# Kernel tuning notes

Hardware: AMD Instinct MI355X
Metric: run time of the kernel (lower is better)

The kernel has to match this reference:

```python
import jax, jax.numpy as jnp
import numpy as np

# ---- module constants (from init_kwargs) ----
VOXEL_SIZE = np.array([0.1, 0.1, 0.2], np.float32)
PC_RANGE = np.array([0.0, -40.0, -3.0, 70.4, 40.0, 1.0], np.float32)
MAX_PTS = 10            # max_points_in_voxel
MAX_VOX = 40000         # max_voxel_num (hard voxelization cap per sample)
GRID = np.round((PC_RANGE[3:] - PC_RANGE[:3]) / VOXEL_SIZE).astype(np.int32)  # [704,800,20] (x,y,z)
BIG = int(GRID[0]) * int(GRID[1]) * int(GRID[2])

PC_MIN = jnp.asarray(PC_RANGE[:3])
VSIZE = jnp.asarray(VOXEL_SIZE)
GRID_J = jnp.asarray(GRID)

B = 8
N_PER_B = 120000


def setup_inputs() -> dict:
    key = jax.random.key(0)
    k1, = jax.random.split(key, 1)
    u = jax.random.uniform(k1, (B * N_PER_B, 4), dtype=jnp.float32)
    # place points inside (and slightly around) pc_range
    x = u[:, 0] * 72.0 - 0.5
    y = u[:, 1] * 82.0 - 41.0
    z = u[:, 2] * 4.4 - 3.2
    inten = u[:, 3]
    bs_idx = jnp.repeat(jnp.arange(B, dtype=jnp.float32), N_PER_B)
    points = jnp.stack([bs_idx, x, y, z, inten], axis=1)  # [960000, 5]
    return {"points": points, "batch_size": B}


def _voxelize_one(pts):
    """Hard voxelization of one point cloud pts [N,4] -> fixed-size buffers.
    Faithful to first-come voxel ordering and per-voxel point caps."""
    N = pts.shape[0]
    idxs = jnp.arange(N, dtype=jnp.int32)
    xyz = pts[:, :3]
    c = jnp.floor((xyz - PC_MIN) / VSIZE).astype(jnp.int32)  # [N,3] (x,y,z)
    valid = jnp.all((c >= 0) & (c < GRID_J), axis=1)
    lid = (c[:, 2] * GRID[1] + c[:, 1]) * GRID[0] + c[:, 0]  # z-major linear id
    lid = jnp.where(valid, lid, BIG)

    order = jnp.argsort(lid)            # stable: within a voxel, original order kept
    lid_s = lid[order]
    is_new = jnp.concatenate([jnp.ones((1,), bool), lid_s[1:] != lid_s[:-1]])
    gid = jnp.cumsum(is_new.astype(jnp.int32)) - 1           # group id per sorted point
    starts = jax.lax.cummax(jnp.where(is_new, idxs, 0))      # group start position
    pos = idxs - starts                                      # rank inside its voxel

    g_lid = jax.ops.segment_min(lid_s, gid, num_segments=N)
    g_valid = g_lid < BIG
    first_orig = jax.ops.segment_min(order.astype(jnp.int32), gid, num_segments=N)
    # voxel slot = first-appearance rank (invalid/empty groups pushed to the end)
    first_key = jnp.where(g_valid, first_orig, N + idxs)
    perm = jnp.argsort(first_key)
    slot = jnp.zeros(N, jnp.int32).at[perm].set(idxs)

    pslot = slot[gid]
    keep = g_valid[gid] & (pslot < MAX_VOX) & (pos < MAX_PTS)
    sslot = jnp.where(keep, pslot, MAX_VOX)   # overflow bucket, sliced off
    spos = jnp.where(keep, pos, 0)
    voxels = jnp.zeros((MAX_VOX + 1, MAX_PTS, pts.shape[1]), pts.dtype)
    voxels = voxels.at[sslot, spos].set(pts[order])[:MAX_VOX]

    gcount = jax.ops.segment_sum(keep.astype(jnp.int32), gid, num_segments=N)
    gslot = jnp.where(g_valid & (slot < MAX_VOX), slot, MAX_VOX)
    num_points = jnp.zeros(MAX_VOX + 1, jnp.int32).at[gslot].set(gcount)[:MAX_VOX]

    cs = c[order]
    gz = jax.ops.segment_min(cs[:, 2], gid, num_segments=N)
    gy = jax.ops.segment_min(cs[:, 1], gid, num_segments=N)
    gx = jax.ops.segment_min(cs[:, 0], gid, num_segments=N)
    coors = jnp.full((MAX_VOX + 1, 3), -1, jnp.int32)
    coors = coors.at[gslot].set(jnp.stack([gz, gy, gx], axis=1))[:MAX_VOX]  # (z,y,x)
    return voxels, num_points, coors


def reference(points, batch_size):
    feats = points[:, 1:]
    n_per_b = feats.shape[0] // batch_size  # points constructed contiguously per sample
    pts = feats.reshape(batch_size, n_per_b, feats.shape[1])
    voxels_b, num_b, coors_b = jax.vmap(_voxelize_one)(pts)
    voxels = voxels_b.reshape(batch_size * MAX_VOX, MAX_PTS, feats.shape[1])
    num_points = num_b.reshape(-1)
    batch_col = jnp.repeat(jnp.arange(batch_size, dtype=jnp.int32), MAX_VOX)[:, None]
    coors_batch = jnp.concatenate([batch_col, coors_b.reshape(-1, 3)], axis=1)  # [b,z,y,x]
    grid_size = jnp.asarray(GRID)
    return voxels, num_points, coors_batch, grid_size
```

## Files before the change

### kernel.cpp

```cpp
#include <hip/hip_runtime.h>

#define NB        8
#define NPB       120000
#define NPTS      (NB * NPB)
#define MAX_PTS   10
#define MAX_VOX   40000
#define GX        704
#define GY        800
#define GZ        20

#define T0        (1 << 18)
#define T0MASK    (T0 - 1)
#define T1        (1 << 16)
#define T1MASK    (T1 - 1)

#define HC2       (1 << 15)
#define HMASK2    (HC2 - 1)
#define NSLOT2    (NB * HC2)

#define TILES     469
#define TILES_PAD 512
#define MBCAP     8192
#define MTILE     2048

#define EMPTY64   0xFFFFFFFFFFFFFFFFull

#define OUT_VOX   0LL
#define OUT_NUM   12800000LL
#define OUT_COOR  13120000LL
#define OUT_GRID  14400000LL

__device__ __forceinline__ bool point_cell(const float* __restrict__ p,
                                           int& cx, int& cy, int& cz) {
    cx = (int)floorf((p[1] - 0.0f)   / 0.1f);
    cy = (int)floorf((p[2] - (-40.0f)) / 0.1f);
    cz = (int)floorf((p[3] - (-3.0f))  / 0.2f);
    return (cx >= 0) & (cx < GX) & (cy >= 0) & (cy < GY) & (cz >= 0) & (cz < GZ);
}

__device__ __forceinline__ unsigned hash0(int lid) {
    return (((unsigned)lid * 2654435761u) >> 14) & T0MASK;
}
__device__ __forceinline__ unsigned hash1(int lid) {
    return (((unsigned)lid * 0x9E3779B1u) >> 16) & T1MASK;
}
__device__ __forceinline__ unsigned slab_hash(int lid) {
    return (((unsigned)lid * 2654435761u) >> 17) & HMASK2;
}

__device__ __forceinline__ void slab_insert(unsigned long long* __restrict__ base,
                                            int lid, int idx) {
    unsigned long long key = ((unsigned long long)(unsigned)lid << 32)
                           | (unsigned long long)(unsigned)idx;
    unsigned h = slab_hash(lid);
    while (true) {
        unsigned long long oo = atomicMin(base + h, key);
        if (oo == EMPTY64) break;
        if ((oo >> 32) == (key >> 32)) break;
        if (oo > key) key = oo;
        h = (h + 1) & HMASK2;
    }
}

__device__ __forceinline__ unsigned slab_find(const unsigned long long* __restrict__ base,
                                              int lid) {
    unsigned h = slab_hash(lid);
    while (true) {
        unsigned long long cur = base[h];
        if ((unsigned)(cur >> 32) == (unsigned)lid) return (unsigned)cur;
        h = (h + 1) & HMASK2;
    }
}

__device__ __forceinline__ unsigned claimer_of(const unsigned* __restrict__ tbl0,
                                               const unsigned* __restrict__ tbl1,
                                               const int* __restrict__ lid32,
                                               int b, int lid) {
    unsigned w = tbl0[b * T0 + hash0(lid)];
    if (lid32[b * NPB + (int)w] == lid) return w;
    w = tbl1[b * T1 + hash1(lid)];
    if (lid32[b * NPB + (int)w] == lid) return w;
    return 0xFFFFFFFFu;
}

__global__ void k_init(const float* __restrict__ pts, float* __restrict__ out,
                       ulonglong2* __restrict__ slab2, unsigned* __restrict__ tbl0,
                       int* __restrict__ lid32, unsigned* __restrict__ mcount) {
    int b = blockIdx.x & 7;
    int idx = (blockIdx.x >> 3) * 256 + threadIdx.x;
    if (idx < NPB) {
        int g = b * NPB + idx;
        const float* p = pts + (long long)g * 5;
        int cx, cy, cz;
        if (point_cell(p, cx, cy, cz)) {
            int lid = (cz * GY + cy) * GX + cx;
            lid32[g] = lid;
            tbl0[b * T0 + hash0(lid)] = (unsigned)idx;
        } else {
            lid32[g] = -1;
        }
    }
    int t = blockIdx.x * 256 + threadIdx.x;
    if (t < NSLOT2 / 2) {
        ulonglong2 e2; e2.x = EMPTY64; e2.y = EMPTY64;
        slab2[t] = e2;
    }
    if (t < NB) mcount[t * 16] = 0u;
    if (t == 0) {
        out[OUT_GRID + 0] = 704.f;
        out[OUT_GRID + 1] = 800.f;
        out[OUT_GRID + 2] = 20.f;
    }
}

__global__ void k_l0(const int* __restrict__ lid32, const unsigned* __restrict__ tbl0,
                     unsigned* __restrict__ tbl1, unsigned char* __restrict__ flag,
                     unsigned long long* __restrict__ slabB) {
    int b = blockIdx.x & 7;
    int idx = (blockIdx.x >> 3) * 256 + threadIdx.x;
    if (idx >= NPB) return;
    int g = b * NPB + idx;
    int lid = lid32[g];
    if (lid < 0) { flag[g] = 0; return; }
    unsigned w = tbl0[b * T0 + hash0(lid)];
    if (lid32[b * NPB + (int)w] == lid) {
        if (w == (unsigned)idx) { flag[g] = 1; return; }
        flag[g] = 0;
        slab_insert(slabB + (size_t)b * HC2, lid, idx);
        return;
    }
    tbl1[b * T1 + hash1(lid)] = (unsigned)idx;
    flag[g] = 2;
}

__global__ void k_l1(const int* __restrict__ lid32, const unsigned* __restrict__ tbl1,
                     unsigned char* __restrict__ flag,
                     unsigned long long* __restrict__ slabB) {
    int b = blockIdx.x & 7;
    int idx = (blockIdx.x >> 3) * 256 + threadIdx.x;
    if (idx >= NPB) return;
    int g = b * NPB + idx;
    if (flag[g] != 2) return;
    int lid = lid32[g];
    unsigned w = tbl1[b * T1 + hash1(lid)];
    if (lid32[b * NPB + (int)w] == lid) {
        if (w == (unsigned)idx) { flag[g] = 1; return; }
        flag[g] = 0;
        slab_insert(slabB + (size_t)b * HC2, lid, idx);
        return;
    }
    flag[g] = 0;
    slab_insert(slabB + (size_t)b * HC2, lid, idx);
}

__global__ void k_sweep(const unsigned long long* __restrict__ slabB,
                        const unsigned* __restrict__ tbl0, const unsigned* __restrict__ tbl1,
                        const int* __restrict__ lid32, unsigned char* __restrict__ flag) {
    int s = blockIdx.x * 256 + threadIdx.x;
    unsigned long long v = slabB[s];
    if (v == EMPTY64) return;
    int b = s >> 15;
    int lid = (int)(unsigned)(v >> 32);
    unsigned smin = (unsigned)v;
    unsigned cl = claimer_of(tbl0, tbl1, lid32, b, lid);
    if (cl == 0xFFFFFFFFu) {
        flag[b * NPB + (int)smin] = 1;
    } else if (smin < cl) {
        flag[b * NPB + (int)cl] = 0;
        flag[b * NPB + (int)smin] = 1;
    }
}

__global__ void k_count(const unsigned* __restrict__ flag32, const int* __restrict__ lid32,
                        const unsigned long long* __restrict__ slabB,
                        const unsigned* __restrict__ tbl0, const unsigned* __restrict__ tbl1,
                        int* __restrict__ tileSum, int2* __restrict__ mlist,
                        unsigned* __restrict__ mcount) {
    int w = blockIdx.x * 4 + ((int)threadIdx.x >> 6);
    int lane = threadIdx.x & 63;
    int b = w & 7;
    int tile = w >> 3;
    int i = tile * 64 + lane;
    unsigned x = 0u;
    if (i < NPB / 4) {
        x = flag32[b * (NPB / 4) + i];
        int4 l4 = ((const int4*)lid32)[b * (NPB / 4) + i];
        #pragma unroll
        for (int k = 0; k < 4; k++) {
            int lk = (k == 0) ? l4.x : (k == 1) ? l4.y : (k == 2) ? l4.z : l4.w;
            if (((x >> (8 * k)) & 255u) == 0u && lk >= 0) {
                unsigned smin = slab_find(slabB + (size_t)b * HC2, lk);
                unsigned cl = claimer_of(tbl0, tbl1, lid32, b, lk);
                unsigned leader = (smin < cl) ? smin : cl;
                int idx = i * 4 + k;
                unsigned m = atomicAdd(&mcount[b * 16], 1u);
                if (m < MBCAP)
                    mlist[(size_t)b * MBCAP + m] = make_int2((int)leader, idx);
            }
        }
    }
    int s = (int)((x * 0x01010101u) >> 24);
    #pragma unroll
    for (int off = 32; off; off >>= 1) s += __shfl_down(s, off);
    if (lane == 0) tileSum[b * TILES_PAD + tile] = s;
}

__global__ void k_finish(const float* __restrict__ pts, const int* __restrict__ lid32,
                         const unsigned char* __restrict__ flag,
                         const int* __restrict__ tileSum,
                         float* __restrict__ out, unsigned short* __restrict__ slotOf) {
    int b = blockIdx.x & 7;
    int tile = blockIdx.x >> 3;
    int t = threadIdx.x;

    __shared__ int sc[256];
    __shared__ int soff[TILES_PAD];
    int v0 = (2 * t     < TILES) ? tileSum[b * TILES_PAD + 2 * t]     : 0;
    int v1 = (2 * t + 1 < TILES) ? tileSum[b * TILES_PAD + 2 * t + 1] : 0;
    int w = v0 + v1;
    sc[t] = w;
    __syncthreads();
    for (int off = 1; off < 256; off <<= 1) {
        int x = sc[t];
        if (t >= off) x += sc[t - off];
        __syncthreads();
        sc[t] = x;
        __syncthreads();
    }
    int e = sc[t] - w;
    soff[2 * t] = e;
    soff[2 * t + 1] = e + v0;
    __syncthreads();

    int idx = tile * 256 + t;
    int g = b * NPB + idx;
    int f = (idx < NPB) ? (int)flag[g] : 0;
    sc[t] = f;
    __syncthreads();
    for (int off = 1; off < 256; off <<= 1) {
        int x = sc[t];
        if (t >= off) x += sc[t - off];
        __syncthreads();
        sc[t] = x;
        __syncthreads();
    }
    int rank = sc[t] - f;

    if (idx >= NPB || !f) return;

    int slot = soff[tile] + rank;
    slotOf[g] = (unsigned short)(slot < 65535 ? slot : 65535);
    if (slot >= MAX_VOX) return;
    int lid = lid32[g];
    unsigned ul = (unsigned)lid;
    unsigned cx = ul % (unsigned)GX;
    unsigned tt = ul / (unsigned)GX;
    unsigned cy = tt % (unsigned)GY;
    unsigned cz = tt / (unsigned)GY;
    long long r = (long long)b * MAX_VOX + slot;
    ((float4*)(out + OUT_COOR))[r] = make_float4((float)b, (float)cz, (float)cy, (float)cx);
    out[OUT_NUM + r] = 1.f;
    const float* p = pts + (long long)g * 5;
    float4* row = (float4*)(out + OUT_VOX) + (size_t)r * MAX_PTS;
    row[0] = make_float4(p[1], p[2], p[3], p[4]);
    float4 zf = make_float4(0.f, 0.f, 0.f, 0.f);
    #pragma unroll
    for (int i = 1; i < MAX_PTS; i++) row[i] = zf;
}

__global__ void k_multi(const float* __restrict__ pts,
                        const int2* __restrict__ mlist, const unsigned* __restrict__ mcount,
                        const unsigned short* __restrict__ slotOf,
                        float* __restrict__ out) {
    int b = blockIdx.y;
    unsigned n = mcount[b * 16];
    if (n > MBCAP) n = MBCAP;
    unsigned t = blockIdx.x * blockDim.x + threadIdx.x;
    const int2* lst = mlist + (size_t)b * MBCAP;
    bool active = (t < n);
    int2 e = active ? lst[t] : make_int2(-1, -1);
    int pos = 1;
    int same = 0;
    __shared__ int2 sm[MTILE];
    for (unsigned chunk = 0; chunk < n; chunk += MTILE) {
        unsigned m = n - chunk;
        if (m > MTILE) m = MTILE;
        for (unsigned i = threadIdx.x; i < m; i += 256)
            sm[i] = lst[chunk + i];
        __syncthreads();
        if (active) {
            #pragma unroll 4
            for (unsigned j = 0; j < m; j++) {
                int2 o = sm[j];
                if (o.x == e.x) { same++; if (o.y < e.y) pos++; }
            }
        }
        __syncthreads();
    }
    if (!active) return;
    int slot = (int)slotOf[(size_t)b * NPB + e.x];
    if (slot >= MAX_VOX) return;
    if (pos == 1) {
        int cnt = same + 1;
        out[OUT_NUM + (long long)b * MAX_VOX + slot] =
            (float)(cnt < MAX_PTS ? cnt : MAX_PTS);
    }
    if (pos >= MAX_PTS) return;
    const float* p = pts + ((long long)b * NPB + e.y) * 5;
    ((float4*)(out + OUT_VOX))[(long long)(b * MAX_VOX + slot) * MAX_PTS + pos] =
        make_float4(p[1], p[2], p[3], p[4]);
}

extern "C" void kernel_launch(void* const* d_in, const int* in_sizes, int n_in,
                              void* d_out, int out_size, void* d_ws, size_t ws_size,
                              hipStream_t stream) {
    const float* pts = (const float*)d_in[0];
    float* out = (float*)d_out;

    char* w = (char*)d_ws;
    unsigned* tbl0 = (unsigned*)w;            w += (size_t)NB * T0 * 4;
    unsigned* tbl1 = (unsigned*)w;            w += (size_t)NB * T1 * 4;
    unsigned long long* slabB = (unsigned long long*)w;
    w += (size_t)NSLOT2 * 8;
    int2* mlist = (int2*)w;  w += (size_t)NB * MBCAP * 8;
    int* lid32 = (int*)w;    w += (size_t)NPTS * 4;
    int* tileSum = (int*)w;  w += (size_t)NB * TILES_PAD * 4;
    unsigned* mcount = (unsigned*)w; w += (size_t)NB * 16 * 4;
    unsigned short* slotOf = (unsigned short*)w; w += (size_t)NPTS * 2;
    unsigned char* flag = (unsigned char*)w;  w += (size_t)NPTS;

    const int PB = TILES * NB;
    k_init<<<dim3(PB), dim3(256), 0, stream>>>(pts, out, (ulonglong2*)slabB,
                                               tbl0, lid32, mcount);
    k_l0<<<dim3(PB), dim3(256), 0, stream>>>(lid32, tbl0, tbl1, flag, slabB);
    k_l1<<<dim3(PB), dim3(256), 0, stream>>>(lid32, tbl1, flag, slabB);
    k_sweep<<<dim3(NSLOT2 / 256), dim3(256), 0, stream>>>(slabB, tbl0, tbl1, lid32, flag);
    k_count<<<dim3(TILES * NB / 4), dim3(256), 0, stream>>>((const unsigned*)flag, lid32,
                                                            slabB, tbl0, tbl1,
                                                            tileSum, mlist, mcount);
    k_finish<<<dim3(PB), dim3(256), 0, stream>>>(pts, lid32, flag, tileSum, out, slotOf);
    k_multi<<<dim3(MBCAP / 256, NB), dim3(256), 0, stream>>>(pts, mlist, mcount, slotOf, out);
}
```

Measured before the change: 156.5 us.

## Drop second-level claim table and use wavefront shuffle scans in finish

The two-level claimer hash tables are replaced by one table twice as large, which removes the k_l1 kernel launch and the second lookup in claimer_of. Points that lose in the single table now fall back to the slab hash, so that table holds more entries and its probe chains get longer. Separately, k_finish's shared-memory Hillis-Steele scans, which synchronise the block at every step, are replaced with wavefront shuffle scans plus a small per-wave sum array. The bigger table also costs more workspace memory and more random-write footprint in k_init.

```diff
diff --git a/kernel.cpp b/kernel.cpp
--- a/kernel.cpp
+++ b/kernel.cpp
@@ -9,10 +9,8 @@
 #define GY        800
 #define GZ        20
 
-#define T0        (1 << 18)
+#define T0        (1 << 19)
 #define T0MASK    (T0 - 1)
-#define T1        (1 << 16)
-#define T1MASK    (T1 - 1)
 
 #define HC2       (1 << 15)
 #define HMASK2    (HC2 - 1)
@@ -39,10 +37,7 @@
 }
 
 __device__ __forceinline__ unsigned hash0(int lid) {
-    return (((unsigned)lid * 2654435761u) >> 14) & T0MASK;
-}
-__device__ __forceinline__ unsigned hash1(int lid) {
-    return (((unsigned)lid * 0x9E3779B1u) >> 16) & T1MASK;
+    return (((unsigned)lid * 2654435761u) >> 13) & T0MASK;
 }
 __device__ __forceinline__ unsigned slab_hash(int lid) {
     return (((unsigned)lid * 2654435761u) >> 17) & HMASK2;
@@ -73,14 +68,27 @@
 }
 
 __device__ __forceinline__ unsigned claimer_of(const unsigned* __restrict__ tbl0,
-                                               const unsigned* __restrict__ tbl1,
                                                const int* __restrict__ lid32,
                                                int b, int lid) {
-    unsigned w = tbl0[b * T0 + hash0(lid)];
-    if (lid32[b * NPB + (int)w] == lid) return w;
-    w = tbl1[b * T1 + hash1(lid)];
+    unsigned w = tbl0[(size_t)b * T0 + hash0(lid)];
     if (lid32[b * NPB + (int)w] == lid) return w;
     return 0xFFFFFFFFu;
+}
+
+__device__ __forceinline__ int block_scan_excl(int v, int t, int* wsum) {
+    int lane = t & 63, wv = t >> 6;
+    int x = v;
+    #pragma unroll
+    for (int d = 1; d < 64; d <<= 1) {
+        int y = __shfl_up(x, d);
+        if (lane >= d) x += y;
+    }
+    if (lane == 63) wsum[wv] = x;
+    __syncthreads();
+    int base = 0;
+    #pragma unroll
+    for (int wj = 0; wj < 3; wj++) if (wj < wv) base += wsum[wj];
+    return base + x - v;
 }
 
 __global__ void k_init(const float* __restrict__ pts, float* __restrict__ out,
@@ -95,7 +103,7 @@
         if (point_cell(p, cx, cy, cz)) {
             int lid = (cz * GY + cy) * GX + cx;
             lid32[g] = lid;
-            tbl0[b * T0 + hash0(lid)] = (unsigned)idx;
+            tbl0[(size_t)b * T0 + hash0(lid)] = (unsigned)idx;
         } else {
             lid32[g] = -1;
         }
@@ -114,7 +122,7 @@
 }
 
 __global__ void k_l0(const int* __restrict__ lid32, const unsigned* __restrict__ tbl0,
-                     unsigned* __restrict__ tbl1, unsigned char* __restrict__ flag,
+                     unsigned char* __restrict__ flag,
                      unsigned long long* __restrict__ slabB) {
     int b = blockIdx.x & 7;
     int idx = (blockIdx.x >> 3) * 256 + threadIdx.x;
@@ -122,39 +130,19 @@
     int g = b * NPB + idx;
     int lid = lid32[g];
     if (lid < 0) { flag[g] = 0; return; }
-    unsigned w = tbl0[b * T0 + hash0(lid)];
+    unsigned w = tbl0[(size_t)b * T0 + hash0(lid)];
     if (lid32[b * NPB + (int)w] == lid) {
         if (w == (unsigned)idx) { flag[g] = 1; return; }
         flag[g] = 0;
         slab_insert(slabB + (size_t)b * HC2, lid, idx);
         return;
     }
-    tbl1[b * T1 + hash1(lid)] = (unsigned)idx;
-    flag[g] = 2;
-}
-
-__global__ void k_l1(const int* __restrict__ lid32, const unsigned* __restrict__ tbl1,
-                     unsigned char* __restrict__ flag,
-                     unsigned long long* __restrict__ slabB) {
-    int b = blockIdx.x & 7;
-    int idx = (blockIdx.x >> 3) * 256 + threadIdx.x;
-    if (idx >= NPB) return;
-    int g = b * NPB + idx;
-    if (flag[g] != 2) return;
-    int lid = lid32[g];
-    unsigned w = tbl1[b * T1 + hash1(lid)];
-    if (lid32[b * NPB + (int)w] == lid) {
-        if (w == (unsigned)idx) { flag[g] = 1; return; }
-        flag[g] = 0;
-        slab_insert(slabB + (size_t)b * HC2, lid, idx);
-        return;
-    }
     flag[g] = 0;
     slab_insert(slabB + (size_t)b * HC2, lid, idx);
 }
 
 __global__ void k_sweep(const unsigned long long* __restrict__ slabB,
-                        const unsigned* __restrict__ tbl0, const unsigned* __restrict__ tbl1,
+                        const unsigned* __restrict__ tbl0,
                         const int* __restrict__ lid32, unsigned char* __restrict__ flag) {
     int s = blockIdx.x * 256 + threadIdx.x;
     unsigned long long v = slabB[s];
@@ -162,7 +150,7 @@
     int b = s >> 15;
     int lid = (int)(unsigned)(v >> 32);
     unsigned smin = (unsigned)v;
-    unsigned cl = claimer_of(tbl0, tbl1, lid32, b, lid);
+    unsigned cl = claimer_of(tbl0, lid32, b, lid);
     if (cl == 0xFFFFFFFFu) {
         flag[b * NPB + (int)smin] = 1;
     } else if (smin < cl) {
@@ -173,7 +161,7 @@
 
 __global__ void k_count(const unsigned* __restrict__ flag32, const int* __restrict__ lid32,
                         const unsigned long long* __restrict__ slabB,
-                        const unsigned* __restrict__ tbl0, const unsigned* __restrict__ tbl1,
+                        const unsigned* __restrict__ tbl0,
                         int* __restrict__ tileSum, int2* __restrict__ mlist,
                         unsigned* __restrict__ mcount) {
     int w = blockIdx.x * 4 + ((int)threadIdx.x >> 6);
@@ -190,7 +178,7 @@
             int lk = (k == 0) ? l4.x : (k == 1) ? l4.y : (k == 2) ? l4.z : l4.w;
             if (((x >> (8 * k)) & 255u) == 0u && lk >= 0) {
                 unsigned smin = slab_find(slabB + (size_t)b * HC2, lk);
-                unsigned cl = claimer_of(tbl0, tbl1, lid32, b, lk);
+                unsigned cl = claimer_of(tbl0, lid32, b, lk);
                 unsigned leader = (smin < cl) ? smin : cl;
                 int idx = i * 4 + k;
                 unsigned m = atomicAdd(&mcount[b * 16], 1u);
@@ -213,38 +201,21 @@
     int tile = blockIdx.x >> 3;
     int t = threadIdx.x;
 
-    __shared__ int sc[256];
+    __shared__ int wsumA[4];
+    __shared__ int wsumB[4];
     __shared__ int soff[TILES_PAD];
     int v0 = (2 * t     < TILES) ? tileSum[b * TILES_PAD + 2 * t]     : 0;
     int v1 = (2 * t + 1 < TILES) ? tileSum[b * TILES_PAD + 2 * t + 1] : 0;
     int w = v0 + v1;
-    sc[t] = w;
-    __syncthreads();
-    for (int off = 1; off < 256; off <<= 1) {
-        int x = sc[t];
-        if (t >= off) x += sc[t - off];
-        __syncthreads();
-        sc[t] = x;
-        __syncthreads();
-    }
-    int e = sc[t] - w;
+    int e = block_scan_excl(w, t, wsumA);
     soff[2 * t] = e;
     soff[2 * t + 1] = e + v0;
-    __syncthreads();
 
     int idx = tile * 256 + t;
     int g = b * NPB + idx;
     int f = (idx < NPB) ? (int)flag[g] : 0;
-    sc[t] = f;
     __syncthreads();
-    for (int off = 1; off < 256; off <<= 1) {
-        int x = sc[t];
-        if (t >= off) x += sc[t - off];
-        __syncthreads();
-        sc[t] = x;
-        __syncthreads();
-    }
-    int rank = sc[t] - f;
+    int rank = block_scan_excl(f, t, wsumB);
 
     if (idx >= NPB || !f) return;
 
@@ -319,7 +290,6 @@
 
     char* w = (char*)d_ws;
     unsigned* tbl0 = (unsigned*)w;            w += (size_t)NB * T0 * 4;
-    unsigned* tbl1 = (unsigned*)w;            w += (size_t)NB * T1 * 4;
     unsigned long long* slabB = (unsigned long long*)w;
     w += (size_t)NSLOT2 * 8;
     int2* mlist = (int2*)w;  w += (size_t)NB * MBCAP * 8;
@@ -332,11 +302,10 @@
     const int PB = TILES * NB;
     k_init<<<dim3(PB), dim3(256), 0, stream>>>(pts, out, (ulonglong2*)slabB,
                                                tbl0, lid32, mcount);
-    k_l0<<<dim3(PB), dim3(256), 0, stream>>>(lid32, tbl0, tbl1, flag, slabB);
-    k_l1<<<dim3(PB), dim3(256), 0, stream>>>(lid32, tbl1, flag, slabB);
-    k_sweep<<<dim3(NSLOT2 / 256), dim3(256), 0, stream>>>(slabB, tbl0, tbl1, lid32, flag);
+    k_l0<<<dim3(PB), dim3(256), 0, stream>>>(lid32, tbl0, flag, slabB);
+    k_sweep<<<dim3(NSLOT2 / 256), dim3(256), 0, stream>>>(slabB, tbl0, lid32, flag);
     k_count<<<dim3(TILES * NB / 4), dim3(256), 0, stream>>>((const unsigned*)flag, lid32,
-                                                            slabB, tbl0, tbl1,
+                                                            slabB, tbl0,
                                                             tileSum, mlist, mcount);
     k_finish<<<dim3(PB), dim3(256), 0, stream>>>(pts, lid32, flag, tileSum, out, slotOf);
     k_multi<<<dim3(MBCAP / 256, NB), dim3(256), 0, stream>>>(pts, mlist, mcount, slotOf, out);
```

New measurement: 156.1 us. No clear change (-0.2%).
